# Kernel optimization log

Measured on AMD Instinct MI355X. Metric: run time of the kernel, lower is better.

## Reference

```python
import jax, jax.numpy as jnp
import numpy as np

TOPK = 50

def setup_inputs() -> dict:
    key = jax.random.key(0)
    k1, k2, k3, k4 = jax.random.split(key, 4)
    B, C, H, W = 8, 64, 256, 256
    x = jax.random.normal(k1, (B, C, H, W), dtype=jnp.float32)
    w_qkv = jax.random.normal(k2, (3 * C, C), dtype=jnp.float32) * 0.05
    w_proj = jax.random.normal(k3, (C, C), dtype=jnp.float32) * 0.05
    b_proj = jax.random.normal(k4, (C,), dtype=jnp.float32) * 0.05
    return {"x": x, "w_qkv": w_qkv, "w_proj": w_proj, "b_proj": b_proj}

def reference(x, w_qkv, w_proj, b_proj):
    B, C, H, W = x.shape
    N = H * W
    scale = C ** -0.5  # num_heads = 1, head_dim = C
    # NOTE: torch does x.reshape(B, N, C) on a (B,C,H,W) tensor -> raw
    # row-major reinterpretation; jnp.reshape matches this exactly.
    xf = x.reshape(B, N, C)
    qkv = xf @ w_qkv.T                                # (B, N, 3C)
    qkv = qkv.reshape(B, N, 3, 1, C).transpose(2, 0, 3, 1, 4)
    q, k, v = qkv[0], qkv[1], qkv[2]                  # each (B, 1, N, C)
    # channel attention: v^T @ k -> (B, 1, C, C)
    attn = jnp.einsum('bhnc,bhnd->bhcd', v, k) * scale
    # top-k mask along last dim (scatter of ones at top-k indices)
    _, idx = jax.lax.top_k(attn, TOPK)                # (B, 1, C, TOPK)
    mask = jax.nn.one_hot(idx, C, dtype=jnp.bool_).any(axis=-2)  # (B,1,C,C)
    attn = jnp.where(mask, attn, -jnp.inf)
    attn = jax.nn.softmax(attn, axis=-1)
    # attn @ q^T -> (B, 1, C, N), then raw reshape to (B, N, C) as in torch
    out = jnp.einsum('bhcd,bhnd->bhcn', attn, q).reshape(B, N, C)
    out = out @ w_proj.T + b_proj
    return out.reshape(B, C, H, W) + x
```

## Files before the change

### kernel.cpp

```cpp
#include <hip/hip_runtime.h>
#include <hip/hip_bf16.h>


#define BATCHES 8
#define NROWS 65536
#define CDIM 64
#define BATCH_FLOATS (NROWS * CDIM)

typedef __attribute__((ext_vector_type(8))) short bf16x8;
typedef __attribute__((ext_vector_type(4))) float f32x4;

__device__ __forceinline__ short f2bf(float f) {
    union { __hip_bfloat16 h; short s; } u;
    u.h = __float2bfloat16(f);
    return u.s;
}
__device__ __forceinline__ unsigned int pk2(float a, float b) {
    return (unsigned int)(unsigned short)f2bf(a) |
           ((unsigned int)(unsigned short)f2bf(b) << 16);
}

__device__ __forceinline__ void fma16g(float a, const float* __restrict__ p, float* acc) {
#pragma unroll
    for (int k = 0; k < 16; ++k) acc[k] = fmaf(a, p[k], acc[k]);
}
__device__ __forceinline__ void fma16v(float a, const float4* p, float* acc) {
    float4 b0 = p[0], b1 = p[1], b2 = p[2], b3 = p[3];
    acc[0]  = fmaf(a, b0.x, acc[0]);  acc[1]  = fmaf(a, b0.y, acc[1]);
    acc[2]  = fmaf(a, b0.z, acc[2]);  acc[3]  = fmaf(a, b0.w, acc[3]);
    acc[4]  = fmaf(a, b1.x, acc[4]);  acc[5]  = fmaf(a, b1.y, acc[5]);
    acc[6]  = fmaf(a, b1.z, acc[6]);  acc[7]  = fmaf(a, b1.w, acc[7]);
    acc[8]  = fmaf(a, b2.x, acc[8]);  acc[9]  = fmaf(a, b2.y, acc[9]);
    acc[10] = fmaf(a, b2.z, acc[10]); acc[11] = fmaf(a, b2.w, acc[11]);
    acc[12] = fmaf(a, b3.x, acc[12]); acc[13] = fmaf(a, b3.y, acc[13]);
    acc[14] = fmaf(a, b3.z, acc[14]); acc[15] = fmaf(a, b3.w, acc[15]);
}

__global__ __launch_bounds__(256) void k0_zero(float* __restrict__ G,
                                               const float* __restrict__ w_proj,
                                               ushort* __restrict__ wpb) {
    int i = blockIdx.x * 256 + threadIdx.x;
    ((float4*)G)[i] = make_float4(0.f, 0.f, 0.f, 0.f);
    if (i < 1024) {
        float4 v = ((const float4*)w_proj)[i];
        uint2 p;
        p.x = pk2(v.x, v.y);
        p.y = pk2(v.z, v.w);
        *(uint2*)(wpb + 4 * i) = p;
    }
}

__global__ __launch_bounds__(256) void k1_gram(const float* __restrict__ x,
                                               float* __restrict__ G,
                                               int ntiles) {
    __shared__ __align__(16) short xt[2][64 * 72];
    int p = blockIdx.x, b = blockIdx.y;
    int tid = threadIdx.x;
    int l = tid & 63;
    int w = tid >> 6;
    int lm = l & 15, q = l >> 4;
    const float* xb = x + (size_t)b * BATCH_FLOATS + (size_t)p * ntiles * 4096;

    f32x4 acc[4];
#pragma unroll
    for (int mi = 0; mi < 4; ++mi) acc[mi] = (f32x4){0.f, 0.f, 0.f, 0.f};

    float4 pre[4];
    {
        const float4* s = (const float4*)xb;
#pragma unroll
        for (int u = 0; u < 4; ++u) pre[u] = s[u * 256 + tid];
    }
    for (int tt = 0; tt < ntiles; ++tt) {
        short* buf = xt[tt & 1];
#pragma unroll
        for (int u = 0; u < 4; ++u) {
            int idx = u * 256 + tid;
            int n = idx >> 4, f = (idx & 15) * 4;
            buf[(f + 0) * 72 + n] = f2bf(pre[u].x);
            buf[(f + 1) * 72 + n] = f2bf(pre[u].y);
            buf[(f + 2) * 72 + n] = f2bf(pre[u].z);
            buf[(f + 3) * 72 + n] = f2bf(pre[u].w);
        }
        if (tt + 1 < ntiles) {
            const float4* s = (const float4*)(xb + (size_t)(tt + 1) * 4096);
#pragma unroll
            for (int u = 0; u < 4; ++u) pre[u] = s[u * 256 + tid];
        }
        __syncthreads();
        bf16x8 bfrag[2];
#pragma unroll
        for (int ks = 0; ks < 2; ++ks)
            bfrag[ks] = *(const bf16x8*)&buf[(16 * w + lm) * 72 + ks * 32 + q * 8];
#pragma unroll
        for (int mi = 0; mi < 4; ++mi) {
#pragma unroll
            for (int ks = 0; ks < 2; ++ks) {
                bf16x8 af = *(const bf16x8*)&buf[(mi * 16 + lm) * 72 + ks * 32 + q * 8];
                acc[mi] = __builtin_amdgcn_mfma_f32_16x16x32_bf16(af, bfrag[ks], acc[mi], 0, 0, 0);
            }
        }
    }
    float* Gb = G + b * 4096;
#pragma unroll
    for (int mi = 0; mi < 4; ++mi)
#pragma unroll
        for (int r = 0; r < 4; ++r)
            atomicAdd(&Gb[(mi * 16 + q * 4 + r) * 64 + 16 * w + lm], acc[mi][r]);
}

#define S68 68
__global__ __launch_bounds__(256) void k2_attn(const float* __restrict__ G,
                                               const float* __restrict__ w_qkv,
                                               ushort* __restrict__ m_bf) {
    __shared__ float A[64 * S68];
    __shared__ float Bf[64 * S68];
    __shared__ float Cf[64 * S68];
    int b = blockIdx.x;
    int tid = threadIdx.x;
    int lane = tid & 63;
    int w = __builtin_amdgcn_readfirstlane(tid >> 6);

    {
        const float4* g4 = (const float4*)(G + b * 4096);
#pragma unroll
        for (int u = 0; u < 4; ++u) {
            int idx = u * 256 + tid;
            int c = idx >> 4, f = (idx & 15) * 4;
            float4 g = g4[idx];
            A[c * S68 + f + 0] = g.x; A[c * S68 + f + 1] = g.y;
            A[c * S68 + f + 2] = g.z; A[c * S68 + f + 3] = g.w;
        }
    }
#pragma unroll
    for (int u = 0; u < 4; ++u) {
        int idx = u * 256 + tid;
        int d = idx >> 4, f = (idx & 15) * 4;
        float4 kv = ((const float4*)(w_qkv + 64 * 64))[idx];
        Bf[(f + 0) * S68 + d] = kv.x; Bf[(f + 1) * S68 + d] = kv.y;
        Bf[(f + 2) * S68 + d] = kv.z; Bf[(f + 3) * S68 + d] = kv.w;
        float4 vv = ((const float4*)(w_qkv + 128 * 64))[idx];
        Cf[(f + 0) * S68 + d] = vv.x; Cf[(f + 1) * S68 + d] = vv.y;
        Cf[(f + 2) * S68 + d] = vv.z; Cf[(f + 3) * S68 + d] = vv.w;
    }
    __syncthreads();

    float acc[16];
#pragma unroll
    for (int k = 0; k < 16; ++k) acc[k] = 0.f;
    for (int f = 0; f < 64; ++f)
        fma16v(A[f * S68 + lane], (const float4*)&Bf[f * S68 + 16 * w], acc);
    __syncthreads();
#pragma unroll
    for (int k = 0; k < 16; ++k) A[lane * S68 + 16 * w + k] = acc[k];
    __syncthreads();

#pragma unroll
    for (int k = 0; k < 16; ++k) acc[k] = 0.f;
    for (int e = 0; e < 64; ++e)
        fma16v(Cf[e * S68 + lane], (const float4*)&A[e * S68 + 16 * w], acc);
#pragma unroll
    for (int k = 0; k < 16; ++k) Bf[lane * S68 + 16 * w + k] = acc[k] * 0.125f;
    __syncthreads();

#pragma unroll 1
    for (int k = 0; k < 16; ++k) {
        int c = 16 * w + k;
        float v = Bf[c * S68 + lane];
        int rank = 0;
#pragma unroll
        for (int d4 = 0; d4 < 16; ++d4) {
            float4 vv = *(const float4*)&Bf[c * S68 + 4 * d4];
            rank += (vv.x > v) || (vv.x == v && (4 * d4 + 0) < lane);
            rank += (vv.y > v) || (vv.y == v && (4 * d4 + 1) < lane);
            rank += (vv.z > v) || (vv.z == v && (4 * d4 + 2) < lane);
            rank += (vv.w > v) || (vv.w == v && (4 * d4 + 3) < lane);
        }
        bool act = rank < 50;
        float mv = act ? v : -INFINITY;
#pragma unroll
        for (int s = 1; s < 64; s <<= 1) mv = fmaxf(mv, __shfl_xor(mv, s, 64));
        float e = act ? expf(v - mv) : 0.f;
        float sum = e;
#pragma unroll
        for (int s = 1; s < 64; s <<= 1) sum += __shfl_xor(sum, s, 64);
        Cf[lane * S68 + c] = e / sum;
    }
    __syncthreads();

#pragma unroll
    for (int k = 0; k < 16; ++k) acc[k] = 0.f;
    for (int d = 0; d < 64; ++d)
        fma16g(Cf[d * S68 + lane], w_qkv + d * 64 + 16 * w, acc);
    unsigned int uu[8];
#pragma unroll
    for (int i = 0; i < 8; ++i)
        uu[i] = pk2(acc[2 * i], acc[2 * i + 1]);
    ushort* dst = m_bf + (size_t)b * 4096 + lane * 64 + 16 * w;
    *(uint4*)dst = make_uint4(uu[0], uu[1], uu[2], uu[3]);
    *(uint4*)(dst + 8) = make_uint4(uu[4], uu[5], uu[6], uu[7]);
}

__global__ __launch_bounds__(256) void k3_main(const float* __restrict__ x,
                                               const ushort* __restrict__ m_bf,
                                               const ushort* __restrict__ wpb,
                                               const float* __restrict__ b_proj,
                                               float* __restrict__ out) {
    __shared__ __align__(16) short xt[64 * 64];
    __shared__ __align__(16) short yyt[64 * 64];
    int t = blockIdx.x, b = blockIdx.y;
    int tid = threadIdx.x;
    int l = tid & 63;
    int w = tid >> 6;
    int lm = l & 15, q = l >> 4;
    const float* xb = x + (size_t)b * BATCH_FLOATS;

    int rowbase = (16 * w + lm) * 1024 + t;
    const float* xr = xb + (size_t)rowbase * 64 + q * 4;
    float4 resid[4];
#pragma unroll
    for (int mi = 0; mi < 4; ++mi) resid[mi] = *(const float4*)(xr + mi * 16);

    const ushort* mb = m_bf + (size_t)b * 4096;
    bf16x8 b1[2];
#pragma unroll
    for (int ks = 0; ks < 2; ++ks)
        b1[ks] = *(const bf16x8*)(mb + (16 * w + lm) * 64 + ks * 32 + q * 8);

    {
        const float4* s = (const float4*)(xb + (size_t)(64 * t) * 64);
#pragma unroll
        for (int u = 0; u < 4; ++u) {
            float4 v = s[u * 256 + tid];
            int row = u * 16 + (tid >> 4);
            int colb = (tid & 15) * 8;
            int off = row * 128 + (colb ^ ((row & 7) << 4));
            uint2 p;
            p.x = pk2(v.x, v.y);
            p.y = pk2(v.z, v.w);
            *(uint2*)((char*)xt + off) = p;
        }
    }
    __syncthreads();

    f32x4 acc1[4];
#pragma unroll
    for (int mi = 0; mi < 4; ++mi) {
        acc1[mi] = (f32x4){0.f, 0.f, 0.f, 0.f};
#pragma unroll
        for (int ks = 0; ks < 2; ++ks) {
            int row = mi * 16 + lm;
            bf16x8 af = *(const bf16x8*)((const char*)xt + row * 128 +
                                         ((ks * 64 + q * 16) ^ ((lm & 7) << 4)));
            acc1[mi] = __builtin_amdgcn_mfma_f32_16x16x32_bf16(af, b1[ks], acc1[mi], 0, 0, 0);
        }
    }
    {
        int r = 16 * w + lm;
#pragma unroll
        for (int mi = 0; mi < 4; ++mi) {
            uint2 p;
            p.x = pk2(acc1[mi][0], acc1[mi][1]);
            p.y = pk2(acc1[mi][2], acc1[mi][3]);
            int off = r * 128 + (((mi * 32) + (q * 8)) ^ ((r & 7) << 4));
            *(uint2*)((char*)yyt + off) = p;
        }
    }

    bf16x8 b2[2];
    {
        int r = 16 * w + lm;
#pragma unroll
        for (int ks = 0; ks < 2; ++ks)
            b2[ks] = *(const bf16x8*)((const char*)yyt + r * 128 +
                                      ((ks * 64 + q * 16) ^ ((r & 7) << 4)));
    }
    f32x4 acc2[4];
#pragma unroll
    for (int mi = 0; mi < 4; ++mi) {
        acc2[mi] = (f32x4){0.f, 0.f, 0.f, 0.f};
#pragma unroll
        for (int ks = 0; ks < 2; ++ks) {
            bf16x8 af = *(const bf16x8*)(wpb + (mi * 16 + lm) * 64 + ks * 32 + q * 8);
            acc2[mi] = __builtin_amdgcn_mfma_f32_16x16x32_bf16(af, b2[ks], acc2[mi], 0, 0, 0);
        }
    }

    float* ob = out + (size_t)b * BATCH_FLOATS + (size_t)rowbase * 64 + q * 4;
#pragma unroll
    for (int mi = 0; mi < 4; ++mi) {
        float4 bias = *(const float4*)(b_proj + mi * 16 + q * 4);
        float4 o;
        o.x = acc2[mi][0] + bias.x + resid[mi].x;
        o.y = acc2[mi][1] + bias.y + resid[mi].y;
        o.z = acc2[mi][2] + bias.z + resid[mi].z;
        o.w = acc2[mi][3] + bias.w + resid[mi].w;
        *(float4*)(ob + mi * 16) = o;
    }
}

extern "C" void kernel_launch(void* const* d_in, const int* in_sizes, int n_in,
                              void* d_out, int out_size, void* d_ws, size_t ws_size,
                              hipStream_t stream) {
    (void)in_sizes; (void)n_in; (void)out_size; (void)ws_size;
    const float* x      = (const float*)d_in[0];
    const float* w_qkv  = (const float*)d_in[1];
    const float* w_proj = (const float*)d_in[2];
    const float* b_proj = (const float*)d_in[3];
    float* out = (float*)d_out;
    float* ws  = (float*)d_ws;

    float*  G    = ws;
    ushort* m_bf = (ushort*)(ws + 32768);
    ushort* wpb  = (ushort*)(ws + 32768 + 16384);

    k0_zero<<<32, 256, 0, stream>>>(G, w_proj, wpb);
    k1_gram<<<dim3(64, BATCHES), 256, 0, stream>>>(x, G, 16);
    k2_attn<<<BATCHES, 256, 0, stream>>>(G, w_qkv, m_bf);
    k3_main<<<dim3(1024, BATCHES), 256, 0, stream>>>(x, m_bf, wpb, b_proj, out);
}
```

Baseline: 349.4 us.

## Replace atomic Gram accumulation with per-block partials reduced in attention kernel

Removes the zeroing kernel and the atomicAdd reduction of per-block Gram tiles. Each block now writes its partial 64x64 Gram to its own workspace slot, and k2_attn sums the 64 partials per batch. The w_proj bf16 conversion moves into k2_attn. The k1 global load pattern also changes so each thread packs bf16 pairs into shared memory with wider stores. The cost is 8 blocks each reading about 1 MB of partials serially, plus uncoalesced-looking scalar loads in k1.

```diff
diff --git a/kernel.cpp b/kernel.cpp
--- a/kernel.cpp
+++ b/kernel.cpp
@@ -36,22 +36,8 @@
     acc[14] = fmaf(a, b3.z, acc[14]); acc[15] = fmaf(a, b3.w, acc[15]);
 }
 
-__global__ __launch_bounds__(256) void k0_zero(float* __restrict__ G,
-                                               const float* __restrict__ w_proj,
-                                               ushort* __restrict__ wpb) {
-    int i = blockIdx.x * 256 + threadIdx.x;
-    ((float4*)G)[i] = make_float4(0.f, 0.f, 0.f, 0.f);
-    if (i < 1024) {
-        float4 v = ((const float4*)w_proj)[i];
-        uint2 p;
-        p.x = pk2(v.x, v.y);
-        p.y = pk2(v.z, v.w);
-        *(uint2*)(wpb + 4 * i) = p;
-    }
-}
-
 __global__ __launch_bounds__(256) void k1_gram(const float* __restrict__ x,
-                                               float* __restrict__ G,
+                                               float* __restrict__ Gpart,
                                                int ntiles) {
     __shared__ __align__(16) short xt[2][64 * 72];
     int p = blockIdx.x, b = blockIdx.y;
@@ -59,33 +45,38 @@
     int l = tid & 63;
     int w = tid >> 6;
     int lm = l & 15, q = l >> 4;
+    int n0 = 4 * (tid >> 4);
+    int c0 = tid & 15;
     const float* xb = x + (size_t)b * BATCH_FLOATS + (size_t)p * ntiles * 4096;
 
     f32x4 acc[4];
 #pragma unroll
     for (int mi = 0; mi < 4; ++mi) acc[mi] = (f32x4){0.f, 0.f, 0.f, 0.f};
 
-    float4 pre[4];
-    {
-        const float4* s = (const float4*)xb;
-#pragma unroll
-        for (int u = 0; u < 4; ++u) pre[u] = s[u * 256 + tid];
-    }
+    float pre[4][4];
+#pragma unroll
+    for (int r = 0; r < 4; ++r)
+#pragma unroll
+        for (int i = 0; i < 4; ++i)
+            pre[r][i] = xb[(size_t)(n0 + r) * 64 + c0 + 16 * i];
+
     for (int tt = 0; tt < ntiles; ++tt) {
         short* buf = xt[tt & 1];
 #pragma unroll
-        for (int u = 0; u < 4; ++u) {
-            int idx = u * 256 + tid;
-            int n = idx >> 4, f = (idx & 15) * 4;
-            buf[(f + 0) * 72 + n] = f2bf(pre[u].x);
-            buf[(f + 1) * 72 + n] = f2bf(pre[u].y);
-            buf[(f + 2) * 72 + n] = f2bf(pre[u].z);
-            buf[(f + 3) * 72 + n] = f2bf(pre[u].w);
+        for (int i = 0; i < 4; ++i) {
+            int f = c0 + 16 * i;
+            uint2 pk;
+            pk.x = pk2(pre[0][i], pre[1][i]);
+            pk.y = pk2(pre[2][i], pre[3][i]);
+            *(uint2*)&buf[f * 72 + n0] = pk;
         }
         if (tt + 1 < ntiles) {
-            const float4* s = (const float4*)(xb + (size_t)(tt + 1) * 4096);
-#pragma unroll
-            for (int u = 0; u < 4; ++u) pre[u] = s[u * 256 + tid];
+            const float* nx = xb + (size_t)(tt + 1) * 4096;
+#pragma unroll
+            for (int r = 0; r < 4; ++r)
+#pragma unroll
+                for (int i = 0; i < 4; ++i)
+                    pre[r][i] = nx[(size_t)(n0 + r) * 64 + c0 + 16 * i];
         }
         __syncthreads();
         bf16x8 bfrag[2];
@@ -101,18 +92,20 @@
             }
         }
     }
-    float* Gb = G + b * 4096;
+    float* Gp = Gpart + ((size_t)(b * 64 + p) << 12);
 #pragma unroll
     for (int mi = 0; mi < 4; ++mi)
 #pragma unroll
         for (int r = 0; r < 4; ++r)
-            atomicAdd(&Gb[(mi * 16 + q * 4 + r) * 64 + 16 * w + lm], acc[mi][r]);
+            Gp[(mi * 16 + q * 4 + r) * 64 + 16 * w + lm] = acc[mi][r];
 }
 
 #define S68 68
-__global__ __launch_bounds__(256) void k2_attn(const float* __restrict__ G,
+__global__ __launch_bounds__(256) void k2_attn(const float* __restrict__ Gpart,
                                                const float* __restrict__ w_qkv,
-                                               ushort* __restrict__ m_bf) {
+                                               const float* __restrict__ w_proj,
+                                               ushort* __restrict__ m_bf,
+                                               ushort* __restrict__ wpb) {
     __shared__ float A[64 * S68];
     __shared__ float Bf[64 * S68];
     __shared__ float Cf[64 * S68];
@@ -121,15 +114,35 @@
     int lane = tid & 63;
     int w = __builtin_amdgcn_readfirstlane(tid >> 6);
 
+    if (tid < 128) {
+        int idx = b * 128 + tid;
+        float4 v = ((const float4*)w_proj)[idx];
+        uint2 pp;
+        pp.x = pk2(v.x, v.y);
+        pp.y = pk2(v.z, v.w);
+        *(uint2*)(wpb + 4 * idx) = pp;
+    }
+
     {
-        const float4* g4 = (const float4*)(G + b * 4096);
+        const float* gp = Gpart + ((size_t)b * 64 << 12);
+        float4 s[4];
+#pragma unroll
+        for (int u = 0; u < 4; ++u) s[u] = make_float4(0.f, 0.f, 0.f, 0.f);
+#pragma unroll 4
+        for (int p = 0; p < 64; ++p) {
+            const float4* g4 = (const float4*)(gp + ((size_t)p << 12));
+#pragma unroll
+            for (int u = 0; u < 4; ++u) {
+                float4 v = g4[u * 256 + tid];
+                s[u].x += v.x; s[u].y += v.y; s[u].z += v.z; s[u].w += v.w;
+            }
+        }
 #pragma unroll
         for (int u = 0; u < 4; ++u) {
             int idx = u * 256 + tid;
             int c = idx >> 4, f = (idx & 15) * 4;
-            float4 g = g4[idx];
-            A[c * S68 + f + 0] = g.x; A[c * S68 + f + 1] = g.y;
-            A[c * S68 + f + 2] = g.z; A[c * S68 + f + 3] = g.w;
+            A[c * S68 + f + 0] = s[u].x; A[c * S68 + f + 1] = s[u].y;
+            A[c * S68 + f + 2] = s[u].z; A[c * S68 + f + 3] = s[u].w;
         }
     }
 #pragma unroll
@@ -310,12 +323,11 @@
     float* out = (float*)d_out;
     float* ws  = (float*)d_ws;
 
-    float*  G    = ws;
-    ushort* m_bf = (ushort*)(ws + 32768);
-    ushort* wpb  = (ushort*)(ws + 32768 + 16384);
-
-    k0_zero<<<32, 256, 0, stream>>>(G, w_proj, wpb);
-    k1_gram<<<dim3(64, BATCHES), 256, 0, stream>>>(x, G, 16);
-    k2_attn<<<BATCHES, 256, 0, stream>>>(G, w_qkv, m_bf);
+    float*  Gpart = ws;
+    ushort* m_bf  = (ushort*)(ws + 8 * 64 * 4096);
+    ushort* wpb   = m_bf + 8 * 4096;
+
+    k1_gram<<<dim3(64, BATCHES), 256, 0, stream>>>(x, Gpart, 16);
+    k2_attn<<<BATCHES, 256, 0, stream>>>(Gpart, w_qkv, w_proj, m_bf, wpb);
     k3_main<<<dim3(1024, BATCHES), 256, 0, stream>>>(x, m_bf, wpb, b_proj, out);
 }
```

Result: slower. 361.6 us (+3.5%).
